# Optimization experiments

Measured on AMD Instinct MI355X. Metric: run time of the kernel, lower is better.

## Reference

```python
import jax, jax.numpy as jnp
import numpy as np

N = 100000   # nodes
E = 1600000  # edges (avg degree 16)
D = 128      # feature / hidden dim
C = 64       # classes
L = 4        # number of GCNII layers
ALPHA = 0.1
LAMDA = 0.5


def setup_inputs() -> dict:
    key = jax.random.key(0)
    ks = jax.random.split(key, 8)
    stdv = 1.0 / np.sqrt(D)
    x = jax.random.normal(ks[0], (N, D), jnp.float32)
    edge_src = jax.random.randint(ks[1], (E,), 0, N)
    edge_dst = jax.random.randint(ks[2], (E,), 0, N)
    edge_weight = jax.random.uniform(ks[3], (E,), jnp.float32)
    w_in = jax.random.uniform(ks[4], (D, D), jnp.float32, -stdv, stdv)
    b_in = jnp.zeros((D,), jnp.float32)
    gcn_w = jax.random.uniform(ks[5], (L, D, D), jnp.float32, -stdv, stdv)
    w_out = jax.random.uniform(ks[6], (D, C), jnp.float32, -stdv, stdv)
    b_out = jnp.zeros((C,), jnp.float32)
    return {"x": x, "edge_src": edge_src, "edge_dst": edge_dst,
            "edge_weight": edge_weight, "w_in": w_in, "b_in": b_in,
            "gcn_w": gcn_w, "w_out": w_out, "b_out": b_out}


def _spmm(edge_src, edge_dst, edge_weight, h):
    # torch.sparse.mm(adj, h): out[i] = sum_j adj[i,j] * h[j]
    # row = dst, col = src in COO terms.
    return jax.ops.segment_sum(edge_weight[:, None] * h[edge_src],
                               edge_dst, num_segments=N)


def reference(x, edge_src, edge_dst, edge_weight, w_in, b_in, gcn_w, w_out, b_out):
    h0 = jax.nn.relu(x @ w_in + b_in)          # [N, D] initial residual
    h = h0
    for l in range(L):
        # GCNConvII called with l_arg = l+1 -> theta = log(lamda/(l_arg+1) + 1)
        theta = float(np.log(LAMDA / (l + 2) + 1.0))
        hi = _spmm(edge_src, edge_dst, edge_weight, h)      # sparse SpMM
        support = (1.0 - ALPHA) * hi + ALPHA * h0           # initial-residual mix
        out = theta * (support @ gcn_w[l]) + (1.0 - theta) * support
        out = out + h                                       # identity residual
        h = jax.nn.relu(out)
    logits = h @ w_out + b_out                              # [N, C]
    return jax.nn.log_softmax(logits, axis=1)
```

## Files before the change

### kernel.cpp

```cpp
#include <hip/hip_runtime.h>
#include <hip/hip_fp16.h>
#include <math.h>

#define N_NODES 100000
#define N_EDGES 1600000
#define DIM     128
#define NCLS    64
#define ALPHA   0.1f

#define NB      391
#define NF      ((size_t)N_NODES * DIM)
#define STRIPES (N_NODES / 16)
#define CHUNK   4096

typedef __attribute__((ext_vector_type(8))) _Float16 f16x8;
typedef __attribute__((ext_vector_type(4))) float    f32x4;

__device__ __forceinline__ __half2 u2h2(unsigned int u) {
    union { unsigned int u; __half2 h; } x; x.u = u; return x.h;
}
__device__ __forceinline__ unsigned int h22u(__half2 h) {
    union { unsigned int u; __half2 h; } x; x.h = h; return x.u;
}


__global__ __launch_bounds__(256) void k_hist(const int* __restrict__ dst,
                                              int* __restrict__ bucket_cnt) {
    __shared__ int hist[NB];
    int t = threadIdx.x;
    for (int b = t; b < NB; b += 256) hist[b] = 0;
    __syncthreads();
    int base = blockIdx.x * CHUNK;
    int end = min(base + CHUNK, N_EDGES);
    for (int i = base + t; i < end; i += 256)
        atomicAdd(&hist[dst[i] >> 8], 1);
    __syncthreads();
    for (int b = t; b < NB; b += 256)
        if (hist[b]) atomicAdd(&bucket_cnt[b], hist[b]);
}

__global__ __launch_bounds__(512) void k_scanb(const int* __restrict__ bucket_cnt,
                                               int* __restrict__ bucket_base,
                                               int* __restrict__ bucket_cursor) {
    __shared__ int s[512];
    int t = threadIdx.x;
    int v = (t < NB) ? bucket_cnt[t] : 0;
    s[t] = v;
    __syncthreads();
    for (int off = 1; off < 512; off <<= 1) {
        int u = (t >= off) ? s[t - off] : 0;
        __syncthreads();
        s[t] += u;
        __syncthreads();
    }
    if (t < NB) {
        int base = s[t] - v;
        bucket_base[t] = base;
        bucket_cursor[t] = base;
    }
    if (t == 0) bucket_base[NB] = N_EDGES;
}

__global__ __launch_bounds__(256) void k_part(const int* __restrict__ src,
                                              const int* __restrict__ dst,
                                              const float* __restrict__ ew,
                                              int* __restrict__ bucket_cursor,
                                              int2* __restrict__ ebuf) {
    __shared__ int lhist[NB], gbase[NB];
    int t = threadIdx.x;
    for (int b = t; b < NB; b += 256) lhist[b] = 0;
    __syncthreads();
    int base = blockIdx.x * CHUNK;
    int end = min(base + CHUNK, N_EDGES);
    for (int i = base + t; i < end; i += 256)
        atomicAdd(&lhist[dst[i] >> 8], 1);
    __syncthreads();
    for (int b = t; b < NB; b += 256) {
        int c = lhist[b];
        gbase[b] = c ? atomicAdd(&bucket_cursor[b], c) : 0;
        lhist[b] = 0;
    }
    __syncthreads();
    for (int i = base + t; i < end; i += 256) {
        int d = dst[i];
        int b = d >> 8;
        int r = atomicAdd(&lhist[b], 1);
        ebuf[gbase[b] + r] = make_int2(src[i] | ((d & 255) << 17),
                                       __float_as_int((1.0f - ALPHA) * ew[i]));
    }
}

__global__ __launch_bounds__(256) void k_sortbucket(
    const int2* __restrict__ ebuf, const int* __restrict__ bucket_base,
    int* __restrict__ row_ptr, int2* __restrict__ colw) {
    __shared__ int cnt[256], pref[256], lcur[256];
    int t = threadIdx.x, b = blockIdx.x;
    cnt[t] = 0;
    __syncthreads();
    int beg = bucket_base[b], end = bucket_base[b + 1];
    for (int i = beg + t; i < end; i += 256)
        atomicAdd(&cnt[ebuf[i].x >> 17], 1);
    __syncthreads();
    int v = cnt[t];
    pref[t] = v;
    __syncthreads();
    for (int off = 1; off < 256; off <<= 1) {
        int u = (t >= off) ? pref[t - off] : 0;
        __syncthreads();
        pref[t] += u;
        __syncthreads();
    }
    int excl = pref[t] - v;
    int node = b * 256 + t;
    if (node < N_NODES) row_ptr[node] = beg + excl;
    if (b == 0 && t == 0) row_ptr[N_NODES] = N_EDGES;
    lcur[t] = beg + excl;
    __syncthreads();
    for (int i = beg + t; i < end; i += 256) {
        int2 e = ebuf[i];
        int pos = atomicAdd(&lcur[e.x >> 17], 1);
        unsigned int w2 = h22u(__float2half2_rn(__int_as_float(e.y)));
        colw[pos] = make_int2(e.x & 0x1FFFF, (int)w2);
    }
}

__global__ void k_prepw(const float* __restrict__ gcnw, const float* __restrict__ wout,
                        const float* __restrict__ win, unsigned short* __restrict__ wp) {
    int tid = blockIdx.x * 256 + threadIdx.x;
    if (tid < 65536) {
        int l = tid >> 14;
        int r = tid & 16383;
        int j = r & 7, lane = (r >> 3) & 63, ch = (r >> 9) & 3, nt = r >> 11;
        int n = nt * 16 + (lane & 15);
        int k = ch * 32 + (lane >> 4) * 8 + j;
        wp[tid] = __half_as_ushort(__float2half(gcnw[l * 16384 + k * 128 + n]));
    } else if (tid < 73728) {
        int r = tid - 65536;
        int j = r & 7, lane = (r >> 3) & 63, ch = (r >> 9) & 3, nt = r >> 11;
        int n = nt * 16 + (lane & 15);
        int k = ch * 32 + (lane >> 4) * 8 + j;
        wp[tid] = __half_as_ushort(__float2half(wout[k * 64 + n]));
    } else if (tid < 90112) {
        int r = tid - 73728;
        int j = r & 7, lane = (r >> 3) & 63, ch = (r >> 9) & 3, nt = r >> 11;
        int n = nt * 16 + (lane & 15);
        int k = ch * 32 + (lane >> 4) * 8 + j;
        wp[tid] = __half_as_ushort(__float2half(win[k * 128 + n]));
    }
}

__global__ __launch_bounds__(256, 8) void k_spmm_csr(
    const int* __restrict__ row_ptr, const int2* __restrict__ colw,
    const unsigned short* __restrict__ h, const unsigned short* __restrict__ h0,
    unsigned short* __restrict__ out) {
    int node = blockIdx.x * 4 + (threadIdx.x >> 6);
    if (node >= N_NODES) return;
    int lane = threadIdx.x & 63;
    int slot = lane >> 4;
    int seg  = lane & 15;
    int beg = row_ptr[node], end = row_ptr[node + 1];

    __half2 z2 = __float2half2_rn(0.f);
    __half2 acc2[4] = {z2, z2, z2, z2};
    if (slot == 0) {
        uint4 z = *(const uint4*)(h0 + (size_t)node * DIM + seg * 8);
        __half2 al2 = __float2half2_rn(ALPHA);
        acc2[0] = __hmul2(al2, u2h2(z.x));
        acc2[1] = __hmul2(al2, u2h2(z.y));
        acc2[2] = __hmul2(al2, u2h2(z.z));
        acc2[3] = __hmul2(al2, u2h2(z.w));
    }

    int last = end - 1;
    for (int e = beg; e < end; e += 16) {
        int e0 = e + slot, e1 = e0 + 4, e2 = e0 + 8, e3 = e0 + 12;
        int2 c0 = colw[min(e0, last)];
        int2 c1 = colw[min(e1, last)];
        int2 c2 = colw[min(e2, last)];
        int2 c3 = colw[min(e3, last)];
        uint4 r0 = *(const uint4*)(h + (size_t)c0.x * DIM + seg * 8);
        uint4 r1 = *(const uint4*)(h + (size_t)c1.x * DIM + seg * 8);
        uint4 r2 = *(const uint4*)(h + (size_t)c2.x * DIM + seg * 8);
        uint4 r3 = *(const uint4*)(h + (size_t)c3.x * DIM + seg * 8);
        __half2 w0 = (e0 < end) ? u2h2((unsigned int)c0.y) : z2;
        __half2 w1 = (e1 < end) ? u2h2((unsigned int)c1.y) : z2;
        __half2 w2 = (e2 < end) ? u2h2((unsigned int)c2.y) : z2;
        __half2 w3 = (e3 < end) ? u2h2((unsigned int)c3.y) : z2;
        acc2[0] = __hfma2(w0, u2h2(r0.x), acc2[0]);
        acc2[1] = __hfma2(w0, u2h2(r0.y), acc2[1]);
        acc2[2] = __hfma2(w0, u2h2(r0.z), acc2[2]);
        acc2[3] = __hfma2(w0, u2h2(r0.w), acc2[3]);
        acc2[0] = __hfma2(w1, u2h2(r1.x), acc2[0]);
        acc2[1] = __hfma2(w1, u2h2(r1.y), acc2[1]);
        acc2[2] = __hfma2(w1, u2h2(r1.z), acc2[2]);
        acc2[3] = __hfma2(w1, u2h2(r1.w), acc2[3]);
        acc2[0] = __hfma2(w2, u2h2(r2.x), acc2[0]);
        acc2[1] = __hfma2(w2, u2h2(r2.y), acc2[1]);
        acc2[2] = __hfma2(w2, u2h2(r2.z), acc2[2]);
        acc2[3] = __hfma2(w2, u2h2(r2.w), acc2[3]);
        acc2[0] = __hfma2(w3, u2h2(r3.x), acc2[0]);
        acc2[1] = __hfma2(w3, u2h2(r3.y), acc2[1]);
        acc2[2] = __hfma2(w3, u2h2(r3.z), acc2[2]);
        acc2[3] = __hfma2(w3, u2h2(r3.w), acc2[3]);
    }

    #pragma unroll
    for (int j = 0; j < 4; j++) {
        unsigned int u = __shfl_xor(h22u(acc2[j]), 16);
        acc2[j] = __hadd2(acc2[j], u2h2(u));
        u = __shfl_xor(h22u(acc2[j]), 32);
        acc2[j] = __hadd2(acc2[j], u2h2(u));
    }

    if (slot == 0) {
        *(uint4*)(out + (size_t)node * DIM + seg * 8) =
            make_uint4(h22u(acc2[0]), h22u(acc2[1]), h22u(acc2[2]), h22u(acc2[3]));
    }
}

__global__ __launch_bounds__(256) void k_in_mfma(
    const float* __restrict__ x, const unsigned short* __restrict__ wp,
    const float* __restrict__ b_in, unsigned short* __restrict__ h0) {
    int wave = threadIdx.x >> 6, lane = threadIdx.x & 63;
    int stripe = blockIdx.x * 4 + wave;
    if (stripe >= STRIPES) return;
    int r0 = stripe * 16;
    int m = lane & 15, q = lane >> 4;

    f32x4 acc[8];
    #pragma unroll
    for (int nt = 0; nt < 8; nt++) acc[nt] = (f32x4){0.f, 0.f, 0.f, 0.f};

    const float* xr = x + (size_t)(r0 + m) * DIM + q * 8;
    #pragma unroll
    for (int ch = 0; ch < 4; ch++) {
        float4 a0 = *(const float4*)(xr + ch * 32);
        float4 a1 = *(const float4*)(xr + ch * 32 + 4);
        f16x8 a;
        a[0] = (_Float16)a0.x; a[1] = (_Float16)a0.y;
        a[2] = (_Float16)a0.z; a[3] = (_Float16)a0.w;
        a[4] = (_Float16)a1.x; a[5] = (_Float16)a1.y;
        a[6] = (_Float16)a1.z; a[7] = (_Float16)a1.w;
        #pragma unroll
        for (int nt = 0; nt < 8; nt++) {
            f16x8 b = *(const f16x8*)(wp + (((nt * 4 + ch) * 64 + lane) << 3));
            acc[nt] = __builtin_amdgcn_mfma_f32_16x16x32_f16(a, b, acc[nt], 0, 0, 0);
        }
    }

    #pragma unroll
    for (int nt = 0; nt < 8; nt++) {
        int col = nt * 16 + m;
        float bias = b_in[col];
        #pragma unroll
        for (int r = 0; r < 4; r++) {
            int row = r0 + q * 4 + r;
            h0[(size_t)row * DIM + col] =
                __half_as_ushort(__float2half(fmaxf(acc[nt][r] + bias, 0.f)));
        }
    }
}

__global__ __launch_bounds__(256) void k_layer_mfma(
    const unsigned short* __restrict__ s_in, const unsigned short* __restrict__ hprev,
    const unsigned short* __restrict__ wp, unsigned short* __restrict__ hout,
    float theta) {
    int wave = threadIdx.x >> 6, lane = threadIdx.x & 63;
    int stripe = blockIdx.x * 4 + wave;
    if (stripe >= STRIPES) return;
    int r0 = stripe * 16;
    int m = lane & 15, q = lane >> 4;
    float omt = 1.f - theta;

    f32x4 acc[8];
    #pragma unroll
    for (int nt = 0; nt < 8; nt++) acc[nt] = (f32x4){0.f, 0.f, 0.f, 0.f};

    const unsigned short* arow = s_in + (size_t)(r0 + m) * DIM + q * 8;
    #pragma unroll
    for (int ch = 0; ch < 4; ch++) {
        f16x8 a = *(const f16x8*)(arow + ch * 32);
        #pragma unroll
        for (int nt = 0; nt < 8; nt++) {
            f16x8 b = *(const f16x8*)(wp + (((nt * 4 + ch) * 64 + lane) << 3));
            acc[nt] = __builtin_amdgcn_mfma_f32_16x16x32_f16(a, b, acc[nt], 0, 0, 0);
        }
    }

    #pragma unroll
    for (int nt = 0; nt < 8; nt++) {
        int col = nt * 16 + m;
        #pragma unroll
        for (int r = 0; r < 4; r++) {
            int row = r0 + q * 4 + r;
            size_t idx = (size_t)row * DIM + col;
            float sup = __half2float(__ushort_as_half(s_in[idx]));
            float hp  = __half2float(__ushort_as_half(hprev[idx]));
            float o = theta * acc[nt][r] + omt * sup + hp;
            hout[idx] = __half_as_ushort(__float2half(fmaxf(o, 0.f)));
        }
    }
}

__global__ __launch_bounds__(256) void k_out_mfma(
    const unsigned short* __restrict__ h, const unsigned short* __restrict__ wp,
    const float* __restrict__ bo, float* __restrict__ out) {
    int wave = threadIdx.x >> 6, lane = threadIdx.x & 63;
    int stripe = blockIdx.x * 4 + wave;
    if (stripe >= STRIPES) return;
    int r0 = stripe * 16;
    int m = lane & 15, q = lane >> 4;

    f32x4 acc[4];
    #pragma unroll
    for (int nt = 0; nt < 4; nt++) acc[nt] = (f32x4){0.f, 0.f, 0.f, 0.f};

    const unsigned short* arow = h + (size_t)(r0 + m) * DIM + q * 8;
    #pragma unroll
    for (int ch = 0; ch < 4; ch++) {
        f16x8 a = *(const f16x8*)(arow + ch * 32);
        #pragma unroll
        for (int nt = 0; nt < 4; nt++) {
            f16x8 b = *(const f16x8*)(wp + (((nt * 4 + ch) * 64 + lane) << 3));
            acc[nt] = __builtin_amdgcn_mfma_f32_16x16x32_f16(a, b, acc[nt], 0, 0, 0);
        }
    }

    float v[4][4];
    #pragma unroll
    for (int nt = 0; nt < 4; nt++) {
        float bias = bo[nt * 16 + m];
        #pragma unroll
        for (int r = 0; r < 4; r++) v[nt][r] = acc[nt][r] + bias;
    }
    #pragma unroll
    for (int r = 0; r < 4; r++) {
        float mx = fmaxf(fmaxf(v[0][r], v[1][r]), fmaxf(v[2][r], v[3][r]));
        #pragma unroll
        for (int off = 1; off < 16; off <<= 1) mx = fmaxf(mx, __shfl_xor(mx, off));
        float s = 0.f;
        #pragma unroll
        for (int nt = 0; nt < 4; nt++) s += __expf(v[nt][r] - mx);
        #pragma unroll
        for (int off = 1; off < 16; off <<= 1) s += __shfl_xor(s, off);
        float lse = mx + logf(s);
        int row = r0 + q * 4 + r;
        #pragma unroll
        for (int nt = 0; nt < 4; nt++)
            out[(size_t)row * NCLS + nt * 16 + m] = v[nt][r] - lse;
    }
}

extern "C" void kernel_launch(void* const* d_in, const int* in_sizes, int n_in,
                              void* d_out, int out_size, void* d_ws, size_t ws_size,
                              hipStream_t stream) {
    const float* x    = (const float*)d_in[0];
    const int*   esrc = (const int*)d_in[1];
    const int*   edst = (const int*)d_in[2];
    const float* ew   = (const float*)d_in[3];
    const float* w_in = (const float*)d_in[4];
    const float* b_in = (const float*)d_in[5];
    const float* gcnw = (const float*)d_in[6];
    const float* wout = (const float*)d_in[7];
    const float* bout = (const float*)d_in[8];
    float* out = (float*)d_out;

    unsigned short* h0 = (unsigned short*)d_ws;
    unsigned short* hA = h0 + NF;
    unsigned short* hB = hA + NF;
    unsigned short* hi = hB + NF;
    unsigned short* wp = hi + NF;
    int2* colw = (int2*)(wp + 90112);
    int2* ebuf = colw + N_EDGES;
    int*  row_ptr       = (int*)(ebuf + N_EDGES);
    int*  bucket_cnt    = row_ptr + (N_NODES + 1);
    int*  bucket_base   = bucket_cnt + NB;
    int*  bucket_cursor = bucket_base + (NB + 1);

    const int PART_B = (N_EDGES + CHUNK - 1) / CHUNK;
    const int MFMA_BLOCKS = (STRIPES + 3) / 4;

    k_prepw<<<(90112 + 255) / 256, 256, 0, stream>>>(gcnw, wout, w_in, wp);

    hipMemsetAsync(bucket_cnt, 0, NB * sizeof(int), stream);
    k_hist<<<PART_B, 256, 0, stream>>>(edst, bucket_cnt);
    k_scanb<<<1, 512, 0, stream>>>(bucket_cnt, bucket_base, bucket_cursor);
    k_part<<<PART_B, 256, 0, stream>>>(esrc, edst, ew, bucket_cursor, ebuf);
    k_sortbucket<<<NB, 256, 0, stream>>>(ebuf, bucket_base, row_ptr, colw);

    k_in_mfma<<<MFMA_BLOCKS, 256, 0, stream>>>(x, wp + 73728, b_in, h0);

    const unsigned short* hprev = h0;
    unsigned short* bufs[2] = {hA, hB};
    for (int l = 0; l < 4; l++) {
        float theta = logf(0.5f / (float)(l + 2) + 1.0f);
        k_spmm_csr<<<(N_NODES + 3) / 4, 256, 0, stream>>>(row_ptr, colw, hprev, h0, hi);
        unsigned short* hnew = bufs[l & 1];
        k_layer_mfma<<<MFMA_BLOCKS, 256, 0, stream>>>(hi, hprev, wp + (size_t)l * 16384,
                                                      hnew, theta);
        hprev = hnew;
    }

    k_out_mfma<<<MFMA_BLOCKS, 256, 0, stream>>>(hprev, wp + 65536, bout, out);
}
```

Measured before the change: 544.8 us.

## Fuse SpMM and layer MFMA into one kernel; fold theta mix into weights

Each layer's SpMM aggregation is merged with the dense MFMA transform in one kernel. A block of four waves gathers 16 node rows into a swizzled LDS tile, then each wave computes 32 output columns with MFMA. This removes the intermediate hi buffer round-trip through global memory and one launch per layer. The theta scaling and (1-theta) identity term are folded into the prepacked fp16 weights, so the epilogue only adds the residual. The cost is serialized gathers per wave (4 nodes each), a block barrier, lower occupancy (launch bounds 6), and fp16 rounding of the folded weights.

```diff
diff --git a/kernel.cpp b/kernel.cpp
--- a/kernel.cpp
+++ b/kernel.cpp
@@ -133,7 +133,9 @@
         int j = r & 7, lane = (r >> 3) & 63, ch = (r >> 9) & 3, nt = r >> 11;
         int n = nt * 16 + (lane & 15);
         int k = ch * 32 + (lane >> 4) * 8 + j;
-        wp[tid] = __half_as_ushort(__float2half(gcnw[l * 16384 + k * 128 + n]));
+        float theta = logf(0.5f / (float)(l + 2) + 1.0f);
+        float v = theta * gcnw[l * 16384 + k * 128 + n] + ((k == n) ? (1.f - theta) : 0.f);
+        wp[tid] = __half_as_ushort(__float2half(v));
     } else if (tid < 73728) {
         int r = tid - 65536;
         int j = r & 7, lane = (r >> 3) & 63, ch = (r >> 9) & 3, nt = r >> 11;
@@ -149,72 +151,110 @@
     }
 }
 
-__global__ __launch_bounds__(256, 8) void k_spmm_csr(
+__global__ __launch_bounds__(256, 6) void k_layer_fused(
     const int* __restrict__ row_ptr, const int2* __restrict__ colw,
-    const unsigned short* __restrict__ h, const unsigned short* __restrict__ h0,
-    unsigned short* __restrict__ out) {
-    int node = blockIdx.x * 4 + (threadIdx.x >> 6);
-    if (node >= N_NODES) return;
-    int lane = threadIdx.x & 63;
+    const unsigned short* __restrict__ h,
+    const unsigned short* __restrict__ h0,
+    const unsigned short* __restrict__ wp,
+    unsigned short* __restrict__ hout) {
+    __shared__ unsigned short sup[16 * 128];
+    int wave = threadIdx.x >> 6, lane = threadIdx.x & 63;
     int slot = lane >> 4;
     int seg  = lane & 15;
-    int beg = row_ptr[node], end = row_ptr[node + 1];
+    int r0 = blockIdx.x * 16;
 
     __half2 z2 = __float2half2_rn(0.f);
-    __half2 acc2[4] = {z2, z2, z2, z2};
-    if (slot == 0) {
-        uint4 z = *(const uint4*)(h0 + (size_t)node * DIM + seg * 8);
-        __half2 al2 = __float2half2_rn(ALPHA);
-        acc2[0] = __hmul2(al2, u2h2(z.x));
-        acc2[1] = __hmul2(al2, u2h2(z.y));
-        acc2[2] = __hmul2(al2, u2h2(z.z));
-        acc2[3] = __hmul2(al2, u2h2(z.w));
-    }
-
-    int last = end - 1;
-    for (int e = beg; e < end; e += 16) {
-        int e0 = e + slot, e1 = e0 + 4, e2 = e0 + 8, e3 = e0 + 12;
-        int2 c0 = colw[min(e0, last)];
-        int2 c1 = colw[min(e1, last)];
-        int2 c2 = colw[min(e2, last)];
-        int2 c3 = colw[min(e3, last)];
-        uint4 r0 = *(const uint4*)(h + (size_t)c0.x * DIM + seg * 8);
-        uint4 r1 = *(const uint4*)(h + (size_t)c1.x * DIM + seg * 8);
-        uint4 r2 = *(const uint4*)(h + (size_t)c2.x * DIM + seg * 8);
-        uint4 r3 = *(const uint4*)(h + (size_t)c3.x * DIM + seg * 8);
-        __half2 w0 = (e0 < end) ? u2h2((unsigned int)c0.y) : z2;
-        __half2 w1 = (e1 < end) ? u2h2((unsigned int)c1.y) : z2;
-        __half2 w2 = (e2 < end) ? u2h2((unsigned int)c2.y) : z2;
-        __half2 w3 = (e3 < end) ? u2h2((unsigned int)c3.y) : z2;
-        acc2[0] = __hfma2(w0, u2h2(r0.x), acc2[0]);
-        acc2[1] = __hfma2(w0, u2h2(r0.y), acc2[1]);
-        acc2[2] = __hfma2(w0, u2h2(r0.z), acc2[2]);
-        acc2[3] = __hfma2(w0, u2h2(r0.w), acc2[3]);
-        acc2[0] = __hfma2(w1, u2h2(r1.x), acc2[0]);
-        acc2[1] = __hfma2(w1, u2h2(r1.y), acc2[1]);
-        acc2[2] = __hfma2(w1, u2h2(r1.z), acc2[2]);
-        acc2[3] = __hfma2(w1, u2h2(r1.w), acc2[3]);
-        acc2[0] = __hfma2(w2, u2h2(r2.x), acc2[0]);
-        acc2[1] = __hfma2(w2, u2h2(r2.y), acc2[1]);
-        acc2[2] = __hfma2(w2, u2h2(r2.z), acc2[2]);
-        acc2[3] = __hfma2(w2, u2h2(r2.w), acc2[3]);
-        acc2[0] = __hfma2(w3, u2h2(r3.x), acc2[0]);
-        acc2[1] = __hfma2(w3, u2h2(r3.y), acc2[1]);
-        acc2[2] = __hfma2(w3, u2h2(r3.z), acc2[2]);
-        acc2[3] = __hfma2(w3, u2h2(r3.w), acc2[3]);
-    }
-
-    #pragma unroll
-    for (int j = 0; j < 4; j++) {
-        unsigned int u = __shfl_xor(h22u(acc2[j]), 16);
-        acc2[j] = __hadd2(acc2[j], u2h2(u));
-        u = __shfl_xor(h22u(acc2[j]), 32);
-        acc2[j] = __hadd2(acc2[j], u2h2(u));
-    }
-
-    if (slot == 0) {
-        *(uint4*)(out + (size_t)node * DIM + seg * 8) =
-            make_uint4(h22u(acc2[0]), h22u(acc2[1]), h22u(acc2[2]), h22u(acc2[3]));
+    __half2 al2 = __float2half2_rn(ALPHA);
+
+    for (int i = 0; i < 4; i++) {
+        int n_loc = wave * 4 + i;
+        int node = r0 + n_loc;
+        int beg = row_ptr[node], end = row_ptr[node + 1];
+
+        __half2 acc2[4] = {z2, z2, z2, z2};
+        if (slot == 0) {
+            uint4 z = *(const uint4*)(h0 + (size_t)node * DIM + seg * 8);
+            acc2[0] = __hmul2(al2, u2h2(z.x));
+            acc2[1] = __hmul2(al2, u2h2(z.y));
+            acc2[2] = __hmul2(al2, u2h2(z.z));
+            acc2[3] = __hmul2(al2, u2h2(z.w));
+        }
+
+        int last = end - 1;
+        for (int e = beg; e < end; e += 16) {
+            int e0 = e + slot, e1 = e0 + 4, e2 = e0 + 8, e3 = e0 + 12;
+            int2 c0 = colw[min(e0, last)];
+            int2 c1 = colw[min(e1, last)];
+            int2 c2 = colw[min(e2, last)];
+            int2 c3 = colw[min(e3, last)];
+            uint4 r0v = *(const uint4*)(h + (size_t)c0.x * DIM + seg * 8);
+            uint4 r1v = *(const uint4*)(h + (size_t)c1.x * DIM + seg * 8);
+            uint4 r2v = *(const uint4*)(h + (size_t)c2.x * DIM + seg * 8);
+            uint4 r3v = *(const uint4*)(h + (size_t)c3.x * DIM + seg * 8);
+            __half2 w0 = (e0 < end) ? u2h2((unsigned int)c0.y) : z2;
+            __half2 w1 = (e1 < end) ? u2h2((unsigned int)c1.y) : z2;
+            __half2 w2 = (e2 < end) ? u2h2((unsigned int)c2.y) : z2;
+            __half2 w3 = (e3 < end) ? u2h2((unsigned int)c3.y) : z2;
+            acc2[0] = __hfma2(w0, u2h2(r0v.x), acc2[0]);
+            acc2[1] = __hfma2(w0, u2h2(r0v.y), acc2[1]);
+            acc2[2] = __hfma2(w0, u2h2(r0v.z), acc2[2]);
+            acc2[3] = __hfma2(w0, u2h2(r0v.w), acc2[3]);
+            acc2[0] = __hfma2(w1, u2h2(r1v.x), acc2[0]);
+            acc2[1] = __hfma2(w1, u2h2(r1v.y), acc2[1]);
+            acc2[2] = __hfma2(w1, u2h2(r1v.z), acc2[2]);
+            acc2[3] = __hfma2(w1, u2h2(r1v.w), acc2[3]);
+            acc2[0] = __hfma2(w2, u2h2(r2v.x), acc2[0]);
+            acc2[1] = __hfma2(w2, u2h2(r2v.y), acc2[1]);
+            acc2[2] = __hfma2(w2, u2h2(r2v.z), acc2[2]);
+            acc2[3] = __hfma2(w2, u2h2(r2v.w), acc2[3]);
+            acc2[0] = __hfma2(w3, u2h2(r3v.x), acc2[0]);
+            acc2[1] = __hfma2(w3, u2h2(r3v.y), acc2[1]);
+            acc2[2] = __hfma2(w3, u2h2(r3v.z), acc2[2]);
+            acc2[3] = __hfma2(w3, u2h2(r3v.w), acc2[3]);
+        }
+
+        #pragma unroll
+        for (int j = 0; j < 4; j++) {
+            unsigned int u = __shfl_xor(h22u(acc2[j]), 16);
+            acc2[j] = __hadd2(acc2[j], u2h2(u));
+            u = __shfl_xor(h22u(acc2[j]), 32);
+            acc2[j] = __hadd2(acc2[j], u2h2(u));
+        }
+
+        if (slot == 0) {
+            int g = seg ^ n_loc;
+            *(uint4*)(sup + n_loc * 128 + g * 8) =
+                make_uint4(h22u(acc2[0]), h22u(acc2[1]), h22u(acc2[2]), h22u(acc2[3]));
+        }
+    }
+    __syncthreads();
+
+    int m = lane & 15, q = lane >> 4;
+    f32x4 acc[2];
+    acc[0] = (f32x4){0.f, 0.f, 0.f, 0.f};
+    acc[1] = (f32x4){0.f, 0.f, 0.f, 0.f};
+    #pragma unroll
+    for (int ch = 0; ch < 4; ch++) {
+        int g = (4 * ch + q) ^ m;
+        f16x8 a = *(const f16x8*)(sup + m * 128 + g * 8);
+        #pragma unroll
+        for (int t2 = 0; t2 < 2; t2++) {
+            int nt = wave * 2 + t2;
+            f16x8 b = *(const f16x8*)(wp + (((nt * 4 + ch) * 64 + lane) << 3));
+            acc[t2] = __builtin_amdgcn_mfma_f32_16x16x32_f16(a, b, acc[t2], 0, 0, 0);
+        }
+    }
+    #pragma unroll
+    for (int t2 = 0; t2 < 2; t2++) {
+        int col = (wave * 2 + t2) * 16 + m;
+        #pragma unroll
+        for (int r = 0; r < 4; r++) {
+            int row = r0 + q * 4 + r;
+            size_t idx = (size_t)row * DIM + col;
+            float hp = __half2float(__ushort_as_half(h[idx]));
+            float o = acc[t2][r] + hp;
+            hout[idx] = __half_as_ushort(__float2half(fmaxf(o, 0.f)));
+        }
     }
 }
 
@@ -257,47 +297,6 @@
             int row = r0 + q * 4 + r;
             h0[(size_t)row * DIM + col] =
                 __half_as_ushort(__float2half(fmaxf(acc[nt][r] + bias, 0.f)));
-        }
-    }
-}
-
-__global__ __launch_bounds__(256) void k_layer_mfma(
-    const unsigned short* __restrict__ s_in, const unsigned short* __restrict__ hprev,
-    const unsigned short* __restrict__ wp, unsigned short* __restrict__ hout,
-    float theta) {
-    int wave = threadIdx.x >> 6, lane = threadIdx.x & 63;
-    int stripe = blockIdx.x * 4 + wave;
-    if (stripe >= STRIPES) return;
-    int r0 = stripe * 16;
-    int m = lane & 15, q = lane >> 4;
-    float omt = 1.f - theta;
-
-    f32x4 acc[8];
-    #pragma unroll
-    for (int nt = 0; nt < 8; nt++) acc[nt] = (f32x4){0.f, 0.f, 0.f, 0.f};
-
-    const unsigned short* arow = s_in + (size_t)(r0 + m) * DIM + q * 8;
-    #pragma unroll
-    for (int ch = 0; ch < 4; ch++) {
-        f16x8 a = *(const f16x8*)(arow + ch * 32);
-        #pragma unroll
-        for (int nt = 0; nt < 8; nt++) {
-            f16x8 b = *(const f16x8*)(wp + (((nt * 4 + ch) * 64 + lane) << 3));
-            acc[nt] = __builtin_amdgcn_mfma_f32_16x16x32_f16(a, b, acc[nt], 0, 0, 0);
-        }
-    }
-
-    #pragma unroll
-    for (int nt = 0; nt < 8; nt++) {
-        int col = nt * 16 + m;
-        #pragma unroll
-        for (int r = 0; r < 4; r++) {
-            int row = r0 + q * 4 + r;
-            size_t idx = (size_t)row * DIM + col;
-            float sup = __half2float(__ushort_as_half(s_in[idx]));
-            float hp  = __half2float(__ushort_as_half(hprev[idx]));
-            float o = theta * acc[nt][r] + omt * sup + hp;
-            hout[idx] = __half_as_ushort(__float2half(fmaxf(o, 0.f)));
         }
     }
 }
@@ -368,8 +367,7 @@
     unsigned short* h0 = (unsigned short*)d_ws;
     unsigned short* hA = h0 + NF;
     unsigned short* hB = hA + NF;
-    unsigned short* hi = hB + NF;
-    unsigned short* wp = hi + NF;
+    unsigned short* wp = hB + NF;
     int2* colw = (int2*)(wp + 90112);
     int2* ebuf = colw + N_EDGES;
     int*  row_ptr       = (int*)(ebuf + N_EDGES);
@@ -393,11 +391,9 @@
     const unsigned short* hprev = h0;
     unsigned short* bufs[2] = {hA, hB};
     for (int l = 0; l < 4; l++) {
-        float theta = logf(0.5f / (float)(l + 2) + 1.0f);
-        k_spmm_csr<<<(N_NODES + 3) / 4, 256, 0, stream>>>(row_ptr, colw, hprev, h0, hi);
         unsigned short* hnew = bufs[l & 1];
-        k_layer_mfma<<<MFMA_BLOCKS, 256, 0, stream>>>(hi, hprev, wp + (size_t)l * 16384,
-                                                      hnew, theta);
+        k_layer_fused<<<STRIPES, 256, 0, stream>>>(row_ptr, colw, hprev, h0,
+                                                   wp + (size_t)l * 16384, hnew);
         hprev = hnew;
     }
 
```

New measurement: 487.0 us. -10.6%, faster.
